# Kernel tuning notes

Measured on AMD Instinct MI355X. Metric: run time of the kernel, lower is better.

## Reference

```python
import jax, jax.numpy as jnp
import numpy as np

DIM = 2048
N_HEADS = 16
N_KV_HEADS = 4
HEAD_DIM = DIM // N_HEADS


def setup_inputs() -> dict:
    key = jax.random.key(0)
    k1, k2, k3, k4, k5 = jax.random.split(key, 5)
    B, T = 2, 2048
    scale = 1.0 / np.sqrt(DIM)
    x = jax.random.normal(k1, (B, T, DIM), dtype=jnp.float32)
    # weights stored as [in, out] so forward is x @ W (same math as nn.Linear)
    Wq = jax.random.normal(k2, (DIM, DIM), dtype=jnp.float32) * scale
    Wk = jax.random.normal(k3, (DIM, N_KV_HEADS * HEAD_DIM), dtype=jnp.float32) * scale
    Wv = jax.random.normal(k4, (DIM, N_KV_HEADS * HEAD_DIM), dtype=jnp.float32) * scale
    Wo = jax.random.normal(k5, (DIM, DIM), dtype=jnp.float32) * scale
    return {"x": x, "Wq": Wq, "Wk": Wk, "Wv": Wv, "Wo": Wo}


def reference(x, Wq, Wk, Wv, Wo):
    B, T, C = x.shape
    G = N_HEADS // N_KV_HEADS  # query heads per kv head
    # projections
    q = (x @ Wq).reshape(B, T, N_KV_HEADS, G, HEAD_DIM)   # [B,T,K,G,d]
    k = (x @ Wk).reshape(B, T, N_KV_HEADS, HEAD_DIM)      # [B,T,K,d]
    v = (x @ Wv).reshape(B, T, N_KV_HEADS, HEAD_DIM)      # [B,T,K,d]
    # attention scores: grouped heads share kv head (no repeat_interleave copy)
    att = jnp.einsum('btkgd,bskd->bkgts', q, k) / np.sqrt(HEAD_DIM)  # [B,K,G,T,T]
    att = jax.nn.softmax(att, axis=-1)
    out = jnp.einsum('bkgts,bskd->btkgd', att, v).reshape(B, T, C)
    return out @ Wo
```

## Files before the change

### kernel.cpp

```cpp
#include <hip/hip_runtime.h>
#include <hip/hip_bf16.h>

typedef __hip_bfloat16 bf16;
typedef __attribute__((ext_vector_type(8))) short short8;
typedef __attribute__((ext_vector_type(4))) short short4v;
typedef __attribute__((ext_vector_type(4))) float f32x4;

#define DIMC 2048
#define TSEQ 2048
#define NB 2
#define KVH 4
#define NH 16
#define HD 128
#define KVD 512
#define QSCALE 0.12751744f

#if __has_builtin(__builtin_amdgcn_exp2f)
#define EXP2(x) __builtin_amdgcn_exp2f(x)
#else
#define EXP2(x) exp2f(x)
#endif

__device__ __forceinline__ void mfma16(f32x4& acc, short8 a, short8 b) {
  acc = __builtin_amdgcn_mfma_f32_16x16x32_bf16(a, b, acc, 0, 0, 0);
}

__device__ __forceinline__ void gload_lds16(const bf16* g, bf16* l) {
  __builtin_amdgcn_global_load_lds(
      (const __attribute__((address_space(1))) void*)g,
      (__attribute__((address_space(3))) void*)l, 16, 0, 0);
}

__device__ __forceinline__ int swz(int row, int col) {
  return col ^ ((row & 7) << 3);
}

__global__ __launch_bounds__(256) void f2b(const float* __restrict__ in,
                                           bf16* __restrict__ out, long n4) {
  long i = (long)blockIdx.x * 256 + threadIdx.x;
  if (i >= n4) return;
  const f32x4 v = *(const f32x4*)(in + i * 4);
  union { short4v s; bf16 h[4]; } u;
#pragma unroll
  for (int j = 0; j < 4; ++j) u.h[j] = __float2bfloat16(v[j]);
  *(short4v*)(out + i * 4) = u.s;
}

__global__ __launch_bounds__(256) void transpose_all(const float* __restrict__ Wq,
                                                     const float* __restrict__ Wk,
                                                     const float* __restrict__ Wv,
                                                     const float* __restrict__ Wo,
                                                     bf16* __restrict__ WT3,
                                                     bf16* __restrict__ WoT) {
  __shared__ bf16 tile[64][72];
  const int y = blockIdx.y;
  const float* in;
  bf16* out;
  int C, rb, cb;
  float scale = 1.0f;
  if (y < 32) {
    in = Wq; out = WT3; C = 2048;
    rb = y * 64; cb = blockIdx.x * 64; scale = QSCALE;
  } else if (y < 40) {
    in = Wk; out = WT3 + (long)2048 * DIMC; C = 512;
    rb = blockIdx.x * 64; cb = (y - 32) * 64;
  } else if (y < 48) {
    in = Wv; out = WT3 + (long)2560 * DIMC; C = 512;
    rb = blockIdx.x * 64; cb = (y - 40) * 64;
  } else {
    in = Wo; out = WoT; C = 2048;
    rb = (y - 48) * 64; cb = blockIdx.x * 64;
  }
  int tx = threadIdx.x & 63, ty = threadIdx.x >> 6;
  for (int i = ty; i < 64; i += 4)
    tile[i][tx] = __float2bfloat16(in[(long)(rb + i) * C + cb + tx] * scale);
  __syncthreads();
  for (int i = ty; i < 64; i += 4)
    out[(long)(cb + i) * DIMC + rb + tx] = tile[tx][i];
}

#define GEMM_BODY(A_, Bt_, K_)                                                  \
  const int tid = threadIdx.x;                                                  \
  const int lane = tid & 63, wid = tid >> 6;                                    \
  const long m0 = blockIdx.y * 128, n0 = blockIdx.x * 128;                      \
  const int wm = (wid >> 1) * 64, wn = (wid & 1) * 64;                          \
  f32x4 acc[4][4] = {};                                                         \
  const int srow = lane >> 2, scol = (lane & 3) * 8;                            \
  const bf16* Ag = A_ + (m0 + srow) * (long)K_ + scol;                          \
  const bf16* Bg = Bt_ + (n0 + srow) * (long)K_ + scol;                         \
  for (int k0 = 0; k0 < K_; k0 += 32) {                                         \
    for (int p = 0; p < 2; ++p) {                                               \
      int rr = p * 64 + wid * 16;                                               \
      gload_lds16(Ag + (long)rr * K_ + k0, As + rr * 32);                       \
      gload_lds16(Bg + (long)rr * K_ + k0, Bs + rr * 32);                       \
    }                                                                           \
    __syncthreads();                                                            \
    const int ko = (lane >> 4) * 8;                                             \
    short8 af[4], bq[4];                                                        \
    _Pragma("unroll") for (int i = 0; i < 4; ++i) {                             \
      af[i] = *(const short8*)(As + (wm + i * 16 + (lane & 15)) * 32 + ko);     \
      bq[i] = *(const short8*)(Bs + (wn + i * 16 + (lane & 15)) * 32 + ko);     \
    }                                                                           \
    _Pragma("unroll") for (int i = 0; i < 4; ++i)                               \
      _Pragma("unroll") for (int j = 0; j < 4; ++j)                             \
        mfma16(acc[i][j], af[i], bq[j]);                                        \
    __syncthreads();                                                            \
  }                                                                             \
  const int cr = (lane >> 4) * 4, cc = lane & 15;

__global__ __launch_bounds__(256) void gemm_qkv(const bf16* __restrict__ A,
                                                const bf16* __restrict__ Bt,
                                                bf16* __restrict__ qp,
                                                bf16* __restrict__ kp,
                                                bf16* __restrict__ vT) {
  __shared__ bf16 As[128 * 32];
  __shared__ bf16 Bs[128 * 32];
  GEMM_BODY(A, Bt, 2048)
#pragma unroll
  for (int i = 0; i < 4; ++i)
#pragma unroll
    for (int j = 0; j < 4; ++j)
#pragma unroll
      for (int r = 0; r < 4; ++r) {
        long m = m0 + wm + i * 16 + cr + r;
        long n = n0 + wn + j * 16 + cc;
        float val = acc[i][j][r];
        if (n0 < 2048) {
          qp[m * DIMC + n] = __float2bfloat16(val);
        } else if (n0 < 2560) {
          kp[m * KVD + (n - 2048)] = __float2bfloat16(val);
        } else {
          long nn = n - 2560;
          long z = (m >> 11) * 4 + (nn >> 7);
          vT[z * (HD * (long)TSEQ) + (nn & 127) * (long)TSEQ + (m & 2047)] =
              __float2bfloat16(val);
        }
      }
}

__global__ __launch_bounds__(256) void gemm_out(const bf16* __restrict__ A,
                                                const bf16* __restrict__ Bt,
                                                float* __restrict__ C) {
  __shared__ bf16 As[128 * 32];
  __shared__ bf16 Bs[128 * 32];
  GEMM_BODY(A, Bt, 2048)
#pragma unroll
  for (int i = 0; i < 4; ++i)
#pragma unroll
    for (int j = 0; j < 4; ++j)
#pragma unroll
      for (int r = 0; r < 4; ++r) {
        long m = m0 + wm + i * 16 + cr + r;
        long n = n0 + wn + j * 16 + cc;
        C[m * DIMC + n] = acc[i][j][r];
      }
}

__global__ __launch_bounds__(256, 2) void attn_fwd(const bf16* __restrict__ Qp,
                                                   const bf16* __restrict__ Kp,
                                                   const bf16* __restrict__ Vt,
                                                   bf16* __restrict__ AO) {
  __shared__ bf16 Ks[2][64 * 128];
  __shared__ bf16 Vts[2][128 * 64];
  const int tid = threadIdx.x;
  const int lane = tid & 63, wid = tid >> 6;
  const int h = blockIdx.y, b = blockIdx.z;
  const int kv = h >> 2;
  const int t0 = blockIdx.x * 128;
  const int lr = lane & 15, lg = lane >> 4;

  short8 aq[2][4];
#pragma unroll
  for (int f = 0; f < 2; ++f) {
    const bf16* qrow =
        Qp + ((long)(b * TSEQ + t0 + wid * 32 + f * 16 + lr)) * DIMC + h * HD + lg * 8;
#pragma unroll
    for (int c = 0; c < 4; ++c) aq[f][c] = *(const short8*)(qrow + c * 32);
  }
  f32x4 o[2][8] = {};
  float mrun[2] = {-1e30f, -1e30f}, lrun[2] = {0.f, 0.f};

  const bf16* Kg = Kp + (long)b * TSEQ * KVD + kv * HD;
  const bf16* Vg = Vt + ((long)(b * KVH + kv)) * HD * TSEQ;

  const int krow = tid >> 2;
  const int vrow = tid >> 1;
  short8 kreg[2][2], vreg[2][2];
#pragma unroll
  for (int s = 0; s < 2; ++s)
#pragma unroll
    for (int p = 0; p < 2; ++p) {
      kreg[s][p] = *(const short8*)(Kg + (long)krow * KVD + (2 * (tid & 3) + s) * 16 + p * 8);
      vreg[s][p] = *(const short8*)(Vg + (long)vrow * TSEQ + (2 * (tid & 1) + s) * 16 + 8 * p);
    }

  for (int s0 = 0; s0 < TSEQ; s0 += 64) {
    const int buf = (s0 >> 6) & 1;
    bf16* Kb = Ks[buf];
    bf16* Vb = Vts[buf];
#pragma unroll
    for (int s = 0; s < 2; ++s)
#pragma unroll
      for (int p = 0; p < 2; ++p) {
        int kc0 = (2 * (tid & 3) + s) * 16;
        *(short8*)(Kb + krow * 128 + swz(krow, kc0 + p * 8)) = kreg[s][p];
        int va = 2 * (tid & 1) + s;
        union { short8 v8; short4v q[2]; } u;
        u.v8 = vreg[s][p];
        int sl1 = (4 * (va >> 1) + 2 * p + vrow) & 7;
        int sl2 = (4 * (va >> 1) + 2 * p + 1 + vrow) & 7;
        int hf = (va & 1) * 4;
        *(short4v*)(Vb + vrow * 64 + sl1 * 8 + hf) = u.q[0];
        *(short4v*)(Vb + vrow * 64 + sl2 * 8 + hf) = u.q[1];
      }
    __syncthreads();
    if (s0 + 64 < TSEQ) {
#pragma unroll
      for (int s = 0; s < 2; ++s)
#pragma unroll
        for (int p = 0; p < 2; ++p) {
          kreg[s][p] = *(const short8*)(Kg + (long)(s0 + 64 + krow) * KVD +
                                        (2 * (tid & 3) + s) * 16 + p * 8);
          vreg[s][p] = *(const short8*)(Vg + (long)vrow * TSEQ + s0 + 64 +
                                        (2 * (tid & 1) + s) * 16 + 8 * p);
        }
    }

    f32x4 sacc[2][4] = {};
    __builtin_amdgcn_s_setprio(1);
#pragma unroll
    for (int sf = 0; sf < 4; ++sf)
#pragma unroll
      for (int c = 0; c < 4; ++c) {
        int row = sf * 16 + lr;
        short8 kf = *(const short8*)(Kb + row * 128 + swz(row, c * 32 + lg * 8));
        mfma16(sacc[0][sf], kf, aq[0][c]);
        mfma16(sacc[1][sf], kf, aq[1][c]);
      }
    __builtin_amdgcn_s_setprio(0);

    union { short8 s; bf16 h[8]; } pb[2][2];
#pragma unroll
    for (int f = 0; f < 2; ++f) {
      float tmax = sacc[f][0][0];
#pragma unroll
      for (int sf = 0; sf < 4; ++sf)
#pragma unroll
        for (int r = 0; r < 4; ++r) tmax = fmaxf(tmax, sacc[f][sf][r]);
      tmax = fmaxf(tmax, __shfl_xor(tmax, 16));
      tmax = fmaxf(tmax, __shfl_xor(tmax, 32));
      if (__any(tmax > mrun[f] + 8.0f)) {
        float mnew = fmaxf(mrun[f], tmax);
        float fac = EXP2(mrun[f] - mnew);
        mrun[f] = mnew;
        lrun[f] *= fac;
#pragma unroll
        for (int df = 0; df < 8; ++df) o[f][df] *= fac;
      }
      float p4[4][4];
      float ps = 0.f;
#pragma unroll
      for (int sf = 0; sf < 4; ++sf)
#pragma unroll
        for (int r = 0; r < 4; ++r) {
          float pv = EXP2(sacc[f][sf][r] - mrun[f]);
          p4[sf][r] = pv;
          ps += pv;
        }
      ps += __shfl_xor(ps, 16);
      ps += __shfl_xor(ps, 32);
      lrun[f] += ps;
#pragma unroll
      for (int c2 = 0; c2 < 2; ++c2)
#pragma unroll
        for (int r = 0; r < 4; ++r) {
          pb[f][c2].h[r] = __float2bfloat16(p4[2 * c2][r]);
          pb[f][c2].h[4 + r] = __float2bfloat16(p4[2 * c2 + 1][r]);
        }
    }

    __builtin_amdgcn_s_setprio(1);
#pragma unroll
    for (int c2 = 0; c2 < 2; ++c2) {
#pragma unroll
      for (int df = 0; df < 8; ++df) {
        int row = df * 16 + lr;
        short8 vf = *(const short8*)(Vb + row * 64 + ((4 * c2 + lg + row) & 7) * 8);
        mfma16(o[0][df], vf, pb[0][c2].s);
        mfma16(o[1][df], vf, pb[1][c2].s);
      }
    }
    __builtin_amdgcn_s_setprio(0);
  }

#pragma unroll
  for (int f = 0; f < 2; ++f) {
    float inv = 1.0f / lrun[f];
    bf16* obase =
        AO + ((long)(b * TSEQ + t0 + wid * 32 + f * 16 + lr)) * DIMC + h * HD + lg * 4;
#pragma unroll
    for (int df = 0; df < 8; ++df) {
      union { short4v s; bf16 h[4]; } ov;
#pragma unroll
      for (int r = 0; r < 4; ++r) ov.h[r] = __float2bfloat16(o[f][df][r] * inv);
      *(short4v*)(obase + df * 16) = ov.s;
    }
  }
}

extern "C" void kernel_launch(void* const* d_in, const int* in_sizes, int n_in,
                              void* d_out, int out_size, void* d_ws, size_t ws_size,
                              hipStream_t stream) {
  const float* x  = (const float*)d_in[0];
  const float* Wq = (const float*)d_in[1];
  const float* Wk = (const float*)d_in[2];
  const float* Wv = (const float*)d_in[3];
  const float* Wo = (const float*)d_in[4];
  float* out = (float*)d_out;
  bf16* ws = (bf16*)d_ws;

  bf16* xb  = ws;
  bf16* WT3 = xb + 8388608;
  bf16* WoT = WT3 + 6291456;
  bf16* qp  = WoT + 4194304;
  bf16* kp  = qp + 8388608;
  bf16* vT  = kp + 2097152;

  f2b<<<8192, 256, 0, stream>>>(x, xb, 2097152);
  transpose_all<<<dim3(32, 80), 256, 0, stream>>>(Wq, Wk, Wv, Wo, WT3, WoT);

  gemm_qkv<<<dim3(24, 32), 256, 0, stream>>>(xb, WT3, qp, kp, vT);

  bf16* ao = xb;
  attn_fwd<<<dim3(16, 16, 2), 256, 0, stream>>>(qp, kp, vT, ao);

  gemm_out<<<dim3(16, 32), 256, 0, stream>>>(ao, WoT, out);
}
```

Baseline: 226.6 us.

## Software-pipeline attention PV matmul one tile behind softmax with triple-buffered V

Restructures the attention inner loop so the P·V MFMAs for the previous KV tile are interleaved with the softmax (max, exp, sum) of the current tile, using a third V shared-memory buffer and carried bf16 P fragments. The goal is to overlap the exp/VALU work with matrix-core work instead of running them back to back. In exchange it uses more LDS (an extra 16KB V buffer) and more registers for the carried P, which may hurt occupancy at the launch bound of 2 blocks. Rescaling of o is now applied after the previous-tile PV accumulation, which keeps the math consistent.

```diff
diff --git a/kernel.cpp b/kernel.cpp
--- a/kernel.cpp
+++ b/kernel.cpp
@@ -161,7 +161,7 @@
                                                    const bf16* __restrict__ Vt,
                                                    bf16* __restrict__ AO) {
   __shared__ bf16 Ks[2][64 * 128];
-  __shared__ bf16 Vts[2][128 * 64];
+  __shared__ bf16 Vts[3][128 * 64];
   const int tid = threadIdx.x;
   const int lane = tid & 63, wid = tid >> 6;
   const int h = blockIdx.y, b = blockIdx.z;
@@ -180,6 +180,16 @@
   f32x4 o[2][8] = {};
   float mrun[2] = {-1e30f, -1e30f}, lrun[2] = {0.f, 0.f};
 
+  union PB { short8 s; bf16 h[8]; };
+  PB pbP[2][2];
+  {
+    short8 z = {0, 0, 0, 0, 0, 0, 0, 0};
+#pragma unroll
+    for (int f = 0; f < 2; ++f)
+#pragma unroll
+      for (int c = 0; c < 2; ++c) pbP[f][c].s = z;
+  }
+
   const bf16* Kg = Kp + (long)b * TSEQ * KVD + kv * HD;
   const bf16* Vg = Vt + ((long)(b * KVH + kv)) * HD * TSEQ;
 
@@ -194,10 +204,11 @@
       vreg[s][p] = *(const short8*)(Vg + (long)vrow * TSEQ + (2 * (tid & 1) + s) * 16 + 8 * p);
     }
 
+  int vw = 0, vp = 2;
   for (int s0 = 0; s0 < TSEQ; s0 += 64) {
-    const int buf = (s0 >> 6) & 1;
-    bf16* Kb = Ks[buf];
-    bf16* Vb = Vts[buf];
+    const int it = s0 >> 6;
+    bf16* Kb = Ks[it & 1];
+    bf16* Vb = Vts[vw];
 #pragma unroll
     for (int s = 0; s < 2; ++s)
 #pragma unroll
@@ -239,58 +250,125 @@
       }
     __builtin_amdgcn_s_setprio(0);
 
-    union { short8 s; bf16 h[8]; } pb[2][2];
-#pragma unroll
-    for (int f = 0; f < 2; ++f) {
-      float tmax = sacc[f][0][0];
-#pragma unroll
-      for (int sf = 0; sf < 4; ++sf)
-#pragma unroll
-        for (int r = 0; r < 4; ++r) tmax = fmaxf(tmax, sacc[f][sf][r]);
-      tmax = fmaxf(tmax, __shfl_xor(tmax, 16));
-      tmax = fmaxf(tmax, __shfl_xor(tmax, 32));
-      if (__any(tmax > mrun[f] + 8.0f)) {
-        float mnew = fmaxf(mrun[f], tmax);
-        float fac = EXP2(mrun[f] - mnew);
-        mrun[f] = mnew;
-        lrun[f] *= fac;
-#pragma unroll
-        for (int df = 0; df < 8; ++df) o[f][df] *= fac;
-      }
-      float p4[4][4];
+    const bf16* Vprev = Vts[vp];
+
+    float tmax0 = sacc[0][0][0];
+#pragma unroll
+    for (int sf = 0; sf < 4; ++sf)
+#pragma unroll
+      for (int r = 0; r < 4; ++r) tmax0 = fmaxf(tmax0, sacc[0][sf][r]);
+    tmax0 = fmaxf(tmax0, __shfl_xor(tmax0, 16));
+    tmax0 = fmaxf(tmax0, __shfl_xor(tmax0, 32));
+    int dor0 = __any(tmax0 > mrun[0] + 8.0f);
+    float fac0 = 1.0f;
+    if (dor0) {
+      float mnew = fmaxf(mrun[0], tmax0);
+      fac0 = EXP2(mrun[0] - mnew);
+      mrun[0] = mnew;
+    }
+
+    if (it > 0) {
+      __builtin_amdgcn_s_setprio(1);
+#pragma unroll
+      for (int df = 0; df < 8; ++df) {
+        int row = df * 16 + lr;
+        short8 vf = *(const short8*)(Vprev + row * 64 + ((lg + row) & 7) * 8);
+        mfma16(o[0][df], vf, pbP[0][0].s);
+        mfma16(o[1][df], vf, pbP[1][0].s);
+      }
+      __builtin_amdgcn_s_setprio(0);
+    }
+
+    PB pbN[2][2];
+    {
       float ps = 0.f;
 #pragma unroll
-      for (int sf = 0; sf < 4; ++sf)
+      for (int c2 = 0; c2 < 2; ++c2)
 #pragma unroll
         for (int r = 0; r < 4; ++r) {
-          float pv = EXP2(sacc[f][sf][r] - mrun[f]);
-          p4[sf][r] = pv;
-          ps += pv;
+          float v0 = EXP2(sacc[0][2 * c2][r] - mrun[0]);
+          float v1 = EXP2(sacc[0][2 * c2 + 1][r] - mrun[0]);
+          ps += v0 + v1;
+          pbN[0][c2].h[r] = __float2bfloat16(v0);
+          pbN[0][c2].h[4 + r] = __float2bfloat16(v1);
         }
       ps += __shfl_xor(ps, 16);
       ps += __shfl_xor(ps, 32);
-      lrun[f] += ps;
-#pragma unroll
-      for (int c2 = 0; c2 < 2; ++c2)
-#pragma unroll
-        for (int r = 0; r < 4; ++r) {
-          pb[f][c2].h[r] = __float2bfloat16(p4[2 * c2][r]);
-          pb[f][c2].h[4 + r] = __float2bfloat16(p4[2 * c2 + 1][r]);
-        }
-    }
-
-    __builtin_amdgcn_s_setprio(1);
-#pragma unroll
-    for (int c2 = 0; c2 < 2; ++c2) {
+      lrun[0] = lrun[0] * fac0 + ps;
+    }
+
+    if (it > 0) {
+      __builtin_amdgcn_s_setprio(1);
 #pragma unroll
       for (int df = 0; df < 8; ++df) {
         int row = df * 16 + lr;
-        short8 vf = *(const short8*)(Vb + row * 64 + ((4 * c2 + lg + row) & 7) * 8);
-        mfma16(o[0][df], vf, pb[0][c2].s);
-        mfma16(o[1][df], vf, pb[1][c2].s);
-      }
-    }
-    __builtin_amdgcn_s_setprio(0);
+        short8 vf = *(const short8*)(Vprev + row * 64 + ((4 + lg + row) & 7) * 8);
+        mfma16(o[0][df], vf, pbP[0][1].s);
+        mfma16(o[1][df], vf, pbP[1][1].s);
+      }
+      __builtin_amdgcn_s_setprio(0);
+    }
+
+    float fac1 = 1.0f;
+    int dor1;
+    {
+      float tmax1 = sacc[1][0][0];
+#pragma unroll
+      for (int sf = 0; sf < 4; ++sf)
+#pragma unroll
+        for (int r = 0; r < 4; ++r) tmax1 = fmaxf(tmax1, sacc[1][sf][r]);
+      tmax1 = fmaxf(tmax1, __shfl_xor(tmax1, 16));
+      tmax1 = fmaxf(tmax1, __shfl_xor(tmax1, 32));
+      dor1 = __any(tmax1 > mrun[1] + 8.0f);
+      if (dor1) {
+        float mnew = fmaxf(mrun[1], tmax1);
+        fac1 = EXP2(mrun[1] - mnew);
+        mrun[1] = mnew;
+      }
+      float ps = 0.f;
+#pragma unroll
+      for (int c2 = 0; c2 < 2; ++c2)
+#pragma unroll
+        for (int r = 0; r < 4; ++r) {
+          float v0 = EXP2(sacc[1][2 * c2][r] - mrun[1]);
+          float v1 = EXP2(sacc[1][2 * c2 + 1][r] - mrun[1]);
+          ps += v0 + v1;
+          pbN[1][c2].h[r] = __float2bfloat16(v0);
+          pbN[1][c2].h[4 + r] = __float2bfloat16(v1);
+        }
+      ps += __shfl_xor(ps, 16);
+      ps += __shfl_xor(ps, 32);
+      lrun[1] = lrun[1] * fac1 + ps;
+    }
+
+    if (dor0) {
+#pragma unroll
+      for (int df = 0; df < 8; ++df) o[0][df] *= fac0;
+    }
+    if (dor1) {
+#pragma unroll
+      for (int df = 0; df < 8; ++df) o[1][df] *= fac1;
+    }
+
+#pragma unroll
+    for (int f = 0; f < 2; ++f)
+#pragma unroll
+      for (int c = 0; c < 2; ++c) pbP[f][c].s = pbN[f][c].s;
+    vp = vw;
+    vw = (vw + 1 == 3) ? 0 : vw + 1;
+  }
+
+  {
+    const bf16* Vprev = Vts[vp];
+#pragma unroll
+    for (int c2 = 0; c2 < 2; ++c2)
+#pragma unroll
+      for (int df = 0; df < 8; ++df) {
+        int row = df * 16 + lr;
+        short8 vf = *(const short8*)(Vprev + row * 64 + ((4 * c2 + lg + row) & 7) * 8);
+        mfma16(o[0][df], vf, pbP[0][c2].s);
+        mfma16(o[1][df], vf, pbP[1][c2].s);
+      }
   }
 
 #pragma unroll
```

Result: no change. 226.7 us (+0.1%).
